# Optimization experiments

Measured on AMD Instinct MI355X. Metric: run time of the kernel, lower is better.

The kernel has to match this reference:

```python
import jax, jax.numpy as jnp
import numpy as np

B, T, F = 2, 128, 88          # batch, time frames, pitch bins (hard-coded 88)
HIDDEN = 64                    # LSTM input dim
N_UNIT = 64                    # channel dim (= 2 * lstm hidden 32)
N_HEAD = 4
HEAD_DIM = N_UNIT // N_HEAD    # 16
WINDOW = 7
N_LAYERS = 2
DIFF_STEPS = 100
LSTM_H = N_UNIT // 2           # 32 per direction


def setup_inputs() -> dict:
    key = jax.random.key(0)
    ks = jax.random.split(key, 12)
    s = 0.05
    inp = {
        'x': jax.random.normal(ks[0], (B, T * F, HIDDEN), jnp.float32),
        't': jax.random.randint(ks[1], (B,), 0, DIFF_STEPS, jnp.int32),
        # LSTM params, stacked [layer, direction, ...]; layer-1 input dim == 2*LSTM_H == HIDDEN
        'lstm_w_ih': s * jax.random.normal(ks[2], (N_LAYERS, 2, 4 * LSTM_H, HIDDEN), jnp.float32),
        'lstm_w_hh': s * jax.random.normal(ks[3], (N_LAYERS, 2, 4 * LSTM_H, LSTM_H), jnp.float32),
        'lstm_b_ih': s * jax.random.normal(ks[4], (N_LAYERS, 2, 4 * LSTM_H), jnp.float32),
        'lstm_b_hh': s * jax.random.normal(ks[5], (N_LAYERS, 2, 4 * LSTM_H), jnp.float32),
        # per-NA-layer params
        't_emb': s * jax.random.normal(ks[6], (N_LAYERS, DIFF_STEPS, N_UNIT), jnp.float32),
        'w_qkv': s * jax.random.normal(ks[7], (N_LAYERS, N_UNIT, 3 * N_UNIT), jnp.float32),
        'b_qkv': jnp.zeros((N_LAYERS, 3 * N_UNIT), jnp.float32),
        'rpb': s * jax.random.normal(ks[8], (N_LAYERS, N_HEAD, 2 * WINDOW - 1, 2 * WINDOW - 1), jnp.float32),
        'w_proj': s * jax.random.normal(ks[9], (N_LAYERS, N_UNIT, N_UNIT), jnp.float32),
        'b_proj': jnp.zeros((N_LAYERS, N_UNIT), jnp.float32),
    }
    return inp


def _lstm_dir(x, w_ih, w_hh, b_ih, b_hh, reverse):
    # x: [N, T, D]; pytorch gate order i, f, g, o
    N = x.shape[0]
    H = w_hh.shape[1]
    xs = jnp.swapaxes(x, 0, 1)
    if reverse:
        xs = xs[::-1]
    b = b_ih + b_hh
    def step(carry, xt):
        h, c = carry
        g = xt @ w_ih.T + h @ w_hh.T + b
        i, f, gg, o = jnp.split(g, 4, axis=-1)
        c = jax.nn.sigmoid(f) * c + jax.nn.sigmoid(i) * jnp.tanh(gg)
        h = jax.nn.sigmoid(o) * jnp.tanh(c)
        return (h, c), h
    h0 = jnp.zeros((N, H), x.dtype)
    _, hs = jax.lax.scan(step, (h0, h0), xs)
    if reverse:
        hs = hs[::-1]
    return jnp.swapaxes(hs, 0, 1)


def _bilstm(x, w_ih, w_hh, b_ih, b_hh):
    for l in range(w_ih.shape[0]):
        fwd = _lstm_dir(x, w_ih[l, 0], w_hh[l, 0], b_ih[l, 0], b_hh[l, 0], False)
        bwd = _lstm_dir(x, w_ih[l, 1], w_hh[l, 1], b_ih[l, 1], b_hh[l, 1], True)
        x = jnp.concatenate([fwd, bwd], axis=-1)
    return x


def _nbh(L, w):
    # NATTEN-style clamped (non-shrinking) neighborhood window per axis
    i = jnp.arange(L)
    start = jnp.clip(i - w // 2, 0, L - w)
    idx = start[:, None] + jnp.arange(w)[None, :]   # [L, w] absolute neighbor idx
    rel = idx - i[:, None] + (w - 1)                # [L, w] rel-pos-bias idx in [0, 2w-2]
    return idx, rel


def _na2d(x, t_idx, emb, wqkv, bqkv, rpb_l, wproj, bproj):
    # x: [B, Th, Tw, C]; diffusion-step conditioning via learned embedding add
    Bx, Th, Tw, C = x.shape
    h = x + emb[t_idx][:, None, None, :]
    qkv = (h @ wqkv + bqkv).reshape(Bx, Th, Tw, 3, N_HEAD, HEAD_DIM)
    q = jnp.moveaxis(qkv[..., 0, :, :], 3, 1) * (HEAD_DIM ** -0.5)  # [B,h,Th,Tw,d]
    k = jnp.moveaxis(qkv[..., 1, :, :], 3, 1)
    v = jnp.moveaxis(qkv[..., 2, :, :], 3, 1)
    ih, rh = _nbh(Th, WINDOW)
    iw, rw = _nbh(Tw, WINDOW)
    # gather windowed neighbors: [B,h,Th,Tw,w,w,d]
    kn = k[:, :, ih[:, None, :, None], iw[None, :, None, :], :]
    vn = v[:, :, ih[:, None, :, None], iw[None, :, None, :], :]
    bias = rpb_l[:, rh[:, None, :, None], rw[None, :, None, :]]     # [h,Th,Tw,w,w]
    logits = jnp.einsum('bhijd,bhijkld->bhijkl', q, kn) + bias[None]
    attn = jax.nn.softmax(logits.reshape(Bx, N_HEAD, Th, Tw, -1), axis=-1).reshape(logits.shape)
    out = jnp.einsum('bhijkl,bhijkld->bhijd', attn, vn)             # [B,h,Th,Tw,d]
    out = jnp.moveaxis(out, 1, 3).reshape(Bx, Th, Tw, C)
    return out @ wproj + bproj


def reference(x, t, lstm_w_ih, lstm_w_hh, lstm_b_ih, lstm_b_hh,
              t_emb, w_qkv, b_qkv, rpb, w_proj, b_proj):
    Bx = x.shape[0]
    Hin = x.shape[-1]
    Tt = x.shape[1] // F
    h = x.reshape(Bx, Tt, F, Hin).transpose(0, 2, 1, 3).reshape(Bx * F, Tt, Hin)
    h = _bilstm(h, lstm_w_ih, lstm_w_hh, lstm_b_ih, lstm_b_hh)      # [B*88, T, n_unit]
    # -> [B, T, 88, n_unit] 2D grid (height=T, width=88)
    h = h.reshape(Bx, F, Tt, N_UNIT).transpose(0, 2, 1, 3)
    for l in range(N_LAYERS):
        h = h + _na2d(h, t, t_emb[l], w_qkv[l], b_qkv[l], rpb[l], w_proj[l], b_proj[l])
    return h
```

## Files before the change

### kernel.cpp

```cpp
#include <hip/hip_runtime.h>
#include <math.h>

#define B_ 2
#define T_ 128
#define F_ 88
#define HID 64
#define NU 64
#define NH 4
#define HD 16
#define LH 32
#define NSEQ (B_*F_)
#define NTOK (B_*T_*F_)
#define NPOS (T_*F_)

__device__ __forceinline__ float fsig(float x) {
    return __builtin_amdgcn_rcpf(1.0f + __expf(-x));
}
__device__ __forceinline__ float ftanh(float x) {
    return 2.0f * __builtin_amdgcn_rcpf(1.0f + __expf(-2.0f*x)) - 1.0f;
}

template<int LAYER>
__global__ void __launch_bounds__(256, 2) gg_kernel(
    const float* __restrict__ xin,
    const float* __restrict__ w_ih,
    const float* __restrict__ b_ih,
    const float* __restrict__ b_hh,
    float* __restrict__ G)
{
    __shared__ __align__(16) float xts[32][68];
    __shared__ __align__(16) float wsh[256][68];
    __shared__ float bsh[256];
    const int s  = blockIdx.x;
    const int t0 = blockIdx.y * 32;
    const int b = s / F_, f = s % F_;
    const int tid = threadIdx.x;

    for (int n = tid; n < 32*64; n += 256) {
        const int tt = n >> 6, k = n & 63;
        xts[tt][k] = (LAYER == 0)
            ? xin[(((size_t)b*T_ + t0+tt)*F_ + f)*HID + k]
            : xin[((size_t)s*T_ + t0+tt)*HID + k];
    }
    for (int n = tid; n < 256*64; n += 256) {
        const int row = n >> 6, k = n & 63;
        wsh[row][k] = w_ih[((size_t)LAYER*256 + row)*HID + k];
    }
    bsh[tid] = b_ih[LAYER*256 + tid] + b_hh[LAYER*256 + tid];
    __syncthreads();

    const int lane = tid & 63;
    const int g    = tid >> 6;
    const int dir  = g >> 1;
    const int th   = g & 1;
    const int rowA = dir*128 + lane;
    const int rowB = dir*128 + 64 + lane;

    float accA[16] = {}, accB[16] = {};
    #pragma unroll 4
    for (int k4 = 0; k4 < 16; k4++) {
        const float4 wA = *(const float4*)&wsh[rowA][k4*4];
        const float4 wB = *(const float4*)&wsh[rowB][k4*4];
        #pragma unroll
        for (int tt = 0; tt < 16; tt++) {
            const float4 xv = *(const float4*)&xts[th*16+tt][k4*4];
            accA[tt] += wA.x*xv.x + wA.y*xv.y + wA.z*xv.z + wA.w*xv.w;
            accB[tt] += wB.x*xv.x + wB.y*xv.y + wB.z*xv.z + wB.w*xv.w;
        }
    }
    const float bA = bsh[rowA], bB = bsh[rowB];
    float2* gout = (float2*)G + ((size_t)(s*2+dir)*T_ + t0 + th*16)*64 + lane;
    #pragma unroll
    for (int tt = 0; tt < 16; tt++) {
        float2 o; o.x = accA[tt] + bA; o.y = accB[tt] + bB;
        gout[(size_t)tt*64] = o;
    }
}

template<int LAYER>
__global__ void __launch_bounds__(128, 1) lstm_rec(
    const float* __restrict__ G,
    const float* __restrict__ w_hh,
    float* __restrict__ outp)
{
    __shared__ float hbuf[T_][NU];
    __shared__ __align__(16) float hstage[2][LH];
    const int s = blockIdx.x;
    const int b = s / F_, f = s % F_;
    const int lane = threadIdx.x & 63;
    const int dir  = threadIdx.x >> 6;

    float2 wh2[LH];
    {
        const float4* pa = (const float4*)(w_hh + ((size_t)(LAYER*2+dir)*128 + lane)*LH);
        const float4* pb = (const float4*)(w_hh + ((size_t)(LAYER*2+dir)*128 + 64 + lane)*LH);
        #pragma unroll
        for (int k4 = 0; k4 < LH/4; k4++) {
            float4 a = pa[k4], c4 = pb[k4];
            wh2[k4*4+0].x=a.x; wh2[k4*4+0].y=c4.x;
            wh2[k4*4+1].x=a.y; wh2[k4*4+1].y=c4.y;
            wh2[k4*4+2].x=a.z; wh2[k4*4+2].y=c4.z;
            wh2[k4*4+3].x=a.w; wh2[k4*4+3].y=c4.w;
        }
    }
    const float2* gp = (const float2*)G + (size_t)(s*2+dir)*T_*64 + lane;
    #define GTIME(st) (dir ? (T_-1-(st)) : (st))

    const float a1 = (lane < LH) ? 2.f : 1.f;
    const float c1 = (lane < LH) ? -1.f : 0.f;

    float h = 0.f, c = 0.f;
    if (lane < LH) hstage[dir][lane] = 0.f;

    #define STEP(gAv, gBv, stepi)                                            \
    {                                                                        \
        float hbc[LH];                                                       \
        _Pragma("unroll")                                                    \
        for (int q = 0; q < LH/4; q++) {                                     \
            const float4 hv = *(const float4*)&hstage[dir][q*4];             \
            hbc[q*4+0]=hv.x; hbc[q*4+1]=hv.y;                                \
            hbc[q*4+2]=hv.z; hbc[q*4+3]=hv.w;                                \
        }                                                                    \
        float aA0 = (gAv), aB0 = (gBv), aA1 = 0.f, aB1 = 0.f;                \
        _Pragma("unroll")                                                    \
        for (int k = 0; k < 16; k++) {                                       \
            aA0 += wh2[k].x*hbc[k];      aB0 += wh2[k].y*hbc[k];             \
            aA1 += wh2[k+16].x*hbc[k+16]; aB1 += wh2[k+16].y*hbc[k+16];      \
        }                                                                    \
        const float accA = aA0 + aA1, accB = aB0 + aB1;                      \
        const float e0 = fsig(accA);                                         \
        const float e1 = fmaf(a1, fsig(a1*accB), c1);                        \
        const float x0 = __shfl_xor(e0, 32, 64);                             \
        const float x1 = __shfl_xor(e1, 32, 64);                             \
        c = x0*c + e0*e1;                                                    \
        h = x1 * ftanh(c);                                                   \
        if (lane < LH) {                                                     \
            hbuf[GTIME(stepi)][dir*LH + lane] = h;                           \
            hstage[dir][lane] = h;                                           \
        }                                                                    \
    }

    float2 A[4], Bf[4];
    #pragma unroll
    for (int i = 0; i < 4; i++) A[i]  = gp[(size_t)GTIME(i)*64];
    #pragma unroll
    for (int i = 0; i < 4; i++) Bf[i] = gp[(size_t)GTIME(4+i)*64];

    #pragma unroll 1
    for (int grp = 0; grp < 32; grp++) {
        float2 P[4];
        const int pf = (grp < 30 ? grp + 2 : 31) * 4;
        #pragma unroll
        for (int i = 0; i < 4; i++) P[i] = gp[(size_t)GTIME(pf+i)*64];
        #pragma unroll
        for (int i = 0; i < 4; i++) { STEP(A[i].x, A[i].y, grp*4 + i); }
        #pragma unroll
        for (int i = 0; i < 4; i++) { A[i] = Bf[i]; Bf[i] = P[i]; }
    }
    #undef STEP
    #undef GTIME
    __syncthreads();

    const int tid = threadIdx.x;
    const float4* lds4 = (const float4*)&hbuf[0][0];
    if (LAYER == 0) {
        float4* out4 = (float4*)outp + (size_t)s*T_*16;
        #pragma unroll
        for (int it = 0; it < 16; it++)
            out4[it*128 + tid] = lds4[it*128 + tid];
    } else {
        const int c4 = tid & 15, trow = tid >> 4;
        #pragma unroll
        for (int it = 0; it < 16; it++) {
            const int t = it*8 + trow;
            ((float4*)outp)[(((size_t)b*T_ + t)*F_ + f)*16 + c4] = lds4[t*16 + c4];
        }
    }
}

__global__ void __launch_bounds__(256, 2) qkv_kernel(
    const float* __restrict__ hcur,
    const int*   __restrict__ tarr,
    const float* __restrict__ t_emb,
    const float* __restrict__ w_qkv,
    const float* __restrict__ b_qkv,
    const int layer,
    float* __restrict__ qb, float* __restrict__ kb, float* __restrict__ vb)
{
    __shared__ float as[64][65];
    __shared__ float wsh[64][64];
    const int m0 = blockIdx.x * 64;
    const int which = blockIdx.y;
    const int tid = threadIdx.x;
    const int bidx = m0 / NPOS;
    const int tb = tarr[bidx];
    const float* embp = t_emb + ((size_t)layer*100 + tb)*HID;

    for (int n = tid; n < 64*64; n += 256) {
        const int mm = n >> 6, k = n & 63;
        as[mm][k]  = hcur[((size_t)m0+mm)*64 + k] + embp[k];
        wsh[mm][k] = w_qkv[((size_t)layer*64 + mm)*192 + which*64 + k];
    }
    __syncthreads();

    const int tm = tid >> 4, tn = tid & 15;
    float acc[4][4] = {};
    for (int k = 0; k < 64; k++) {
        const float a0 = as[tm*4+0][k];
        const float a1 = as[tm*4+1][k];
        const float a2 = as[tm*4+2][k];
        const float a3 = as[tm*4+3][k];
        const float4 w = *(const float4*)&wsh[k][tn*4];
        acc[0][0]+=a0*w.x; acc[0][1]+=a0*w.y; acc[0][2]+=a0*w.z; acc[0][3]+=a0*w.w;
        acc[1][0]+=a1*w.x; acc[1][1]+=a1*w.y; acc[1][2]+=a1*w.z; acc[1][3]+=a1*w.w;
        acc[2][0]+=a2*w.x; acc[2][1]+=a2*w.y; acc[2][2]+=a2*w.z; acc[2][3]+=a2*w.w;
        acc[3][0]+=a3*w.x; acc[3][1]+=a3*w.y; acc[3][2]+=a3*w.z; acc[3][3]+=a3*w.w;
    }

    float* dst = (which == 0) ? qb : (which == 1) ? kb : vb;
    const float scale = (which == 0) ? 0.25f : 1.0f;
    const int hh = tn >> 2;
    const int dbase = (tn & 3) * 4;
    const float4 bv = *(const float4*)&b_qkv[(size_t)layer*192 + which*64 + tn*4];
    #pragma unroll
    for (int r = 0; r < 4; r++) {
        const int row = m0 + tm*4 + r;
        const int pos = row - bidx*NPOS;
        float4 o;
        o.x = (acc[r][0] + bv.x) * scale;
        o.y = (acc[r][1] + bv.y) * scale;
        o.z = (acc[r][2] + bv.z) * scale;
        o.w = (acc[r][3] + bv.w) * scale;
        *(float4*)&dst[(((size_t)bidx*NH + hh)*NPOS + pos)*HD + dbase] = o;
    }
}

__global__ void __launch_bounds__(384, 1) nattn_kernel(
    const float* __restrict__ qb,
    const float* __restrict__ kb,
    const float* __restrict__ vb,
    const float* __restrict__ rpb,
    const int layer,
    float* __restrict__ ao)
{
    __shared__ float kv[2][10][88][20];
    __shared__ float rp[169];
    const int blk = blockIdx.x;
    const int bh = blk & 7;
    const int it = blk >> 3;
    const int i0 = it*4;
    const int h  = bh & 3;
    const int bb = bh >> 2;
    const int tid = threadIdx.x;
    const int rs = min(max(i0-3, 0), T_-10);
    const float* kbase = kb + (size_t)bh*NPOS*HD;
    const float* vbase = vb + (size_t)bh*NPOS*HD;

    const bool act = (tid < 4*F_);
    const int isub = act ? (tid / F_) : 0;
    const int j    = act ? (tid - isub*F_) : 0;
    const int i    = i0 + isub;
    const int ihs  = min(max(i-3, 0), T_-7);
    const int ro   = ihs - rs;
    const int cw   = min(max(j-3, 0), F_-7);

    float4 q0, q1, q2, q3;
    if (act) {
        const float4* qp = (const float4*)&qb[((size_t)bh*NPOS + i*F_ + j)*HD];
        q0 = qp[0]; q1 = qp[1]; q2 = qp[2]; q3 = qp[3];
    }
    for (int n = tid; n < 169; n += 384)
        rp[n] = rpb[((size_t)layer*NH + h)*169 + n];
    for (int n4 = tid; n4 < 10*88*4; n4 += 384) {
        const int d4   = n4 & 3;
        const int rest = n4 >> 2;
        const int c    = rest % 88;
        const int r    = rest / 88;
        const size_t goff = ((size_t)(rs+r)*F_ + c)*HD + d4*4;
        *(float4*)&kv[0][r][c][d4*4] = *(const float4*)&kbase[goff];
        *(float4*)&kv[1][r][c][d4*4] = *(const float4*)&vbase[goff];
    }
    __syncthreads();

    if (act) {
        float lg[49];
        #pragma unroll
        for (int ki = 0; ki < 7; ki++) {
            const int rh = ihs + ki - i + 6;
            #pragma unroll
            for (int kj = 0; kj < 7; kj++) {
                const float4* kp = (const float4*)&kv[0][ro+ki][cw+kj][0];
                const float4 k0 = kp[0], k1 = kp[1], k2 = kp[2], k3 = kp[3];
                float d = q0.x*k0.x + q0.y*k0.y + q0.z*k0.z + q0.w*k0.w
                        + q1.x*k1.x + q1.y*k1.y + q1.z*k1.z + q1.w*k1.w
                        + q2.x*k2.x + q2.y*k2.y + q2.z*k2.z + q2.w*k2.w
                        + q3.x*k3.x + q3.y*k3.y + q3.z*k3.z + q3.w*k3.w;
                lg[ki*7+kj] = d + rp[rh*13 + (cw + kj - j + 6)];
            }
        }
        float m = lg[0];
        #pragma unroll
        for (int n = 1; n < 49; n++) m = fmaxf(m, lg[n]);
        float ssum = 0.f;
        #pragma unroll
        for (int n = 0; n < 49; n++) { lg[n] = __expf(lg[n] - m); ssum += lg[n]; }
        const float inv = __builtin_amdgcn_rcpf(ssum);
        #pragma unroll
        for (int n = 0; n < 49; n++) lg[n] *= inv;

        float4 o0 = {0,0,0,0}, o1 = {0,0,0,0}, o2 = {0,0,0,0}, o3 = {0,0,0,0};
        #pragma unroll
        for (int ki = 0; ki < 7; ki++) {
            #pragma unroll
            for (int kj = 0; kj < 7; kj++) {
                const float a = lg[ki*7+kj];
                const float4* vp = (const float4*)&kv[1][ro+ki][cw+kj][0];
                const float4 v0 = vp[0], v1 = vp[1], v2 = vp[2], v3 = vp[3];
                o0.x += a*v0.x; o0.y += a*v0.y; o0.z += a*v0.z; o0.w += a*v0.w;
                o1.x += a*v1.x; o1.y += a*v1.y; o1.z += a*v1.z; o1.w += a*v1.w;
                o2.x += a*v2.x; o2.y += a*v2.y; o2.z += a*v2.z; o2.w += a*v2.w;
                o3.x += a*v3.x; o3.y += a*v3.y; o3.z += a*v3.z; o3.w += a*v3.w;
            }
        }
        float4* op = (float4*)&ao[(((size_t)bb*T_ + i)*F_ + j)*NU + h*HD];
        op[0]=o0; op[1]=o1; op[2]=o2; op[3]=o3;
    }
}

__global__ void __launch_bounds__(256, 2) proj_kernel(
    const float* __restrict__ ain,
    const float* __restrict__ hres,
    const float* __restrict__ w_proj,
    const float* __restrict__ b_proj,
    const int layer,
    float* __restrict__ outp)
{
    __shared__ float as[64][65];
    __shared__ float wsh[64][64];
    const int m0 = blockIdx.x * 64;
    const int tid = threadIdx.x;
    for (int n = tid; n < 64*64; n += 256) {
        const int mm = n >> 6, k = n & 63;
        as[mm][k]  = ain[((size_t)m0+mm)*64 + k];
        wsh[mm][k] = w_proj[(size_t)layer*4096 + n];
    }
    __syncthreads();
    const int tm = tid >> 4, tn = tid & 15;
    float acc[4][4] = {};
    for (int k = 0; k < 64; k++) {
        const float a0 = as[tm*4+0][k];
        const float a1 = as[tm*4+1][k];
        const float a2 = as[tm*4+2][k];
        const float a3 = as[tm*4+3][k];
        const float4 w = *(const float4*)&wsh[k][tn*4];
        acc[0][0]+=a0*w.x; acc[0][1]+=a0*w.y; acc[0][2]+=a0*w.z; acc[0][3]+=a0*w.w;
        acc[1][0]+=a1*w.x; acc[1][1]+=a1*w.y; acc[1][2]+=a1*w.z; acc[1][3]+=a1*w.w;
        acc[2][0]+=a2*w.x; acc[2][1]+=a2*w.y; acc[2][2]+=a2*w.z; acc[2][3]+=a2*w.w;
        acc[3][0]+=a3*w.x; acc[3][1]+=a3*w.y; acc[3][2]+=a3*w.z; acc[3][3]+=a3*w.w;
    }
    const float4 bv = *(const float4*)&b_proj[(size_t)layer*64 + tn*4];
    #pragma unroll
    for (int r = 0; r < 4; r++) {
        const int row = m0 + tm*4 + r;
        const float4 hv = *(const float4*)&hres[(size_t)row*64 + tn*4];
        float4 o;
        o.x = hv.x + acc[r][0] + bv.x;
        o.y = hv.y + acc[r][1] + bv.y;
        o.z = hv.z + acc[r][2] + bv.z;
        o.w = hv.w + acc[r][3] + bv.w;
        *(float4*)&outp[(size_t)row*64 + tn*4] = o;
    }
}

extern "C" void kernel_launch(void* const* d_in, const int* in_sizes, int n_in,
                              void* d_out, int out_size, void* d_ws, size_t ws_size,
                              hipStream_t stream) {
    const float* x      = (const float*)d_in[0];
    const int*   tarr   = (const int*)  d_in[1];
    const float* w_ih   = (const float*)d_in[2];
    const float* w_hh   = (const float*)d_in[3];
    const float* b_ih   = (const float*)d_in[4];
    const float* b_hh   = (const float*)d_in[5];
    const float* t_emb  = (const float*)d_in[6];
    const float* w_qkv  = (const float*)d_in[7];
    const float* b_qkv  = (const float*)d_in[8];
    const float* rpb    = (const float*)d_in[9];
    const float* w_proj = (const float*)d_in[10];
    const float* b_proj = (const float*)d_in[11];

    float* ws   = (float*)d_ws;
    const size_t CH = (size_t)NTOK * NU;
    float* hcur = ws;
    float* h0   = ws + CH;
    float* G    = ws + 2*CH;
    float* qbuf = ws + 2*CH;
    float* kbuf = ws + 3*CH;
    float* vbuf = ws + 4*CH;
    float* ao   = ws + 5*CH;
    float* outp = (float*)d_out;

    gg_kernel<0><<<dim3(NSEQ, T_/32), 256, 0, stream>>>(x,  w_ih, b_ih, b_hh, G);
    lstm_rec<0><<<NSEQ, 128, 0, stream>>>(G, w_hh, h0);
    gg_kernel<1><<<dim3(NSEQ, T_/32), 256, 0, stream>>>(h0, w_ih, b_ih, b_hh, G);
    lstm_rec<1><<<NSEQ, 128, 0, stream>>>(G, w_hh, hcur);

    for (int l = 0; l < 2; l++) {
        qkv_kernel<<<dim3(NTOK/64, 3), 256, 0, stream>>>(
            hcur, tarr, t_emb, w_qkv, b_qkv, l, qbuf, kbuf, vbuf);
        nattn_kernel<<<(T_/4)*8, 384, 0, stream>>>(
            qbuf, kbuf, vbuf, rpb, l, ao);
        proj_kernel<<<NTOK/64, 256, 0, stream>>>(
            ao, hcur, w_proj, b_proj, l, (l == 0) ? hcur : outp);
    }
}
```

Measured before the change: 241.3 us.

## Fuse LSTM input projection into recurrent kernel with pipelined x staging

Removes the separate gate-precompute kernel and its G buffer round trip through global memory. Each recurrent block now keeps its w_ih rows in registers (128 extra floats per thread) and computes the input projection for future timesteps inside the loop. It stages x through a 4-slot shared ring with one-group-ahead global prefetch, so this work can overlap the serial recurrence. The cost is much higher register pressure and extra ALU work on the latency-bound recurrent path, which runs with only 176 blocks.

```diff
diff --git a/kernel.cpp b/kernel.cpp
--- a/kernel.cpp
+++ b/kernel.cpp
@@ -21,74 +21,37 @@
 }
 
 template<int LAYER>
-__global__ void __launch_bounds__(256, 2) gg_kernel(
+__global__ void __launch_bounds__(128, 1) lstm_fused(
     const float* __restrict__ xin,
     const float* __restrict__ w_ih,
+    const float* __restrict__ w_hh,
     const float* __restrict__ b_ih,
     const float* __restrict__ b_hh,
-    float* __restrict__ G)
-{
-    __shared__ __align__(16) float xts[32][68];
-    __shared__ __align__(16) float wsh[256][68];
-    __shared__ float bsh[256];
-    const int s  = blockIdx.x;
-    const int t0 = blockIdx.y * 32;
-    const int b = s / F_, f = s % F_;
-    const int tid = threadIdx.x;
-
-    for (int n = tid; n < 32*64; n += 256) {
-        const int tt = n >> 6, k = n & 63;
-        xts[tt][k] = (LAYER == 0)
-            ? xin[(((size_t)b*T_ + t0+tt)*F_ + f)*HID + k]
-            : xin[((size_t)s*T_ + t0+tt)*HID + k];
-    }
-    for (int n = tid; n < 256*64; n += 256) {
-        const int row = n >> 6, k = n & 63;
-        wsh[row][k] = w_ih[((size_t)LAYER*256 + row)*HID + k];
-    }
-    bsh[tid] = b_ih[LAYER*256 + tid] + b_hh[LAYER*256 + tid];
-    __syncthreads();
-
-    const int lane = tid & 63;
-    const int g    = tid >> 6;
-    const int dir  = g >> 1;
-    const int th   = g & 1;
-    const int rowA = dir*128 + lane;
-    const int rowB = dir*128 + 64 + lane;
-
-    float accA[16] = {}, accB[16] = {};
-    #pragma unroll 4
-    for (int k4 = 0; k4 < 16; k4++) {
-        const float4 wA = *(const float4*)&wsh[rowA][k4*4];
-        const float4 wB = *(const float4*)&wsh[rowB][k4*4];
-        #pragma unroll
-        for (int tt = 0; tt < 16; tt++) {
-            const float4 xv = *(const float4*)&xts[th*16+tt][k4*4];
-            accA[tt] += wA.x*xv.x + wA.y*xv.y + wA.z*xv.z + wA.w*xv.w;
-            accB[tt] += wB.x*xv.x + wB.y*xv.y + wB.z*xv.z + wB.w*xv.w;
-        }
-    }
-    const float bA = bsh[rowA], bB = bsh[rowB];
-    float2* gout = (float2*)G + ((size_t)(s*2+dir)*T_ + t0 + th*16)*64 + lane;
-    #pragma unroll
-    for (int tt = 0; tt < 16; tt++) {
-        float2 o; o.x = accA[tt] + bA; o.y = accB[tt] + bB;
-        gout[(size_t)tt*64] = o;
-    }
-}
-
-template<int LAYER>
-__global__ void __launch_bounds__(128, 1) lstm_rec(
-    const float* __restrict__ G,
-    const float* __restrict__ w_hh,
     float* __restrict__ outp)
 {
     __shared__ float hbuf[T_][NU];
     __shared__ __align__(16) float hstage[2][LH];
+    __shared__ __align__(16) float xstage[2][4][4][64];
     const int s = blockIdx.x;
     const int b = s / F_, f = s % F_;
     const int lane = threadIdx.x & 63;
     const int dir  = threadIdx.x >> 6;
+
+    float wA[64], wB[64];
+    {
+        const float* wbase = w_ih + (size_t)((LAYER*2+dir)*128)*HID;
+        const float4* pa = (const float4*)(wbase + (size_t)lane*HID);
+        const float4* pb = (const float4*)(wbase + (size_t)(64+lane)*HID);
+        #pragma unroll
+        for (int q = 0; q < 16; q++) {
+            float4 a = pa[q], bq = pb[q];
+            wA[q*4+0]=a.x;  wA[q*4+1]=a.y;  wA[q*4+2]=a.z;  wA[q*4+3]=a.w;
+            wB[q*4+0]=bq.x; wB[q*4+1]=bq.y; wB[q*4+2]=bq.z; wB[q*4+3]=bq.w;
+        }
+    }
+    const int brow = (LAYER*2+dir)*128;
+    const float biasA = b_ih[brow + lane]      + b_hh[brow + lane];
+    const float biasB = b_ih[brow + 64 + lane] + b_hh[brow + 64 + lane];
 
     float2 wh2[LH];
     {
@@ -103,14 +66,41 @@
             wh2[k4*4+3].x=a.w; wh2[k4*4+3].y=c4.w;
         }
     }
-    const float2* gp = (const float2*)G + (size_t)(s*2+dir)*T_*64 + lane;
-    #define GTIME(st) (dir ? (T_-1-(st)) : (st))
 
     const float a1 = (lane < LH) ? 2.f : 1.f;
     const float c1 = (lane < LH) ? -1.f : 0.f;
-
     float h = 0.f, c = 0.f;
     if (lane < LH) hstage[dir][lane] = 0.f;
+
+    #define GTIME(st) (dir ? (T_-1-(st)) : (st))
+    const int xtt = lane >> 4;
+    const int xk4 = (lane & 15) * 4;
+    #define XADDR(t) ((LAYER==0) ? ((((size_t)b*T_+(t))*F_ + f)*HID + xk4) \
+                                 : (((size_t)s*T_+(t))*HID + xk4))
+    #define LOADX(g) (*(const float4*)&xin[XADDR(GTIME(min((g)*4+xtt, T_-1)))])
+    #define STOREX(slot, v) { *(float4*)&xstage[dir][slot][xtt][xk4] = (v); }
+
+    #define PRODUCE(slot, GA, GB)                                            \
+    {                                                                        \
+        _Pragma("unroll")                                                    \
+        for (int tt = 0; tt < 4; tt++) {                                     \
+            float pa0 = biasA, pb0 = biasB, pa1 = 0.f, pb1 = 0.f;            \
+            _Pragma("unroll")                                                \
+            for (int q = 0; q < 8; q++) {                                    \
+                const float4 xv = *(const float4*)&xstage[dir][slot][tt][q*8];   \
+                const float4 xw = *(const float4*)&xstage[dir][slot][tt][q*8+4]; \
+                pa0 += wA[q*8+0]*xv.x + wA[q*8+1]*xv.y                       \
+                     + wA[q*8+2]*xv.z + wA[q*8+3]*xv.w;                      \
+                pb0 += wB[q*8+0]*xv.x + wB[q*8+1]*xv.y                       \
+                     + wB[q*8+2]*xv.z + wB[q*8+3]*xv.w;                      \
+                pa1 += wA[q*8+4]*xw.x + wA[q*8+5]*xw.y                       \
+                     + wA[q*8+6]*xw.z + wA[q*8+7]*xw.w;                      \
+                pb1 += wB[q*8+4]*xw.x + wB[q*8+5]*xw.y                       \
+                     + wB[q*8+6]*xw.z + wB[q*8+7]*xw.w;                      \
+            }                                                                \
+            GA[tt] = pa0 + pa1; GB[tt] = pb0 + pb1;                          \
+        }                                                                    \
+    }
 
     #define STEP(gAv, gBv, stepi)                                            \
     {                                                                        \
@@ -140,24 +130,33 @@
         }                                                                    \
     }
 
-    float2 A[4], Bf[4];
-    #pragma unroll
-    for (int i = 0; i < 4; i++) A[i]  = gp[(size_t)GTIME(i)*64];
-    #pragma unroll
-    for (int i = 0; i < 4; i++) Bf[i] = gp[(size_t)GTIME(4+i)*64];
+    {
+        float4 t0 = LOADX(0), t1 = LOADX(1), t2 = LOADX(2);
+        STOREX(0, t0); STOREX(1, t1); STOREX(2, t2);
+    }
+    float AA[4], AB[4], BA[4], BB[4];
+    PRODUCE(0, AA, AB);
+    PRODUCE(1, BA, BB);
+    float4 xreg = LOADX(3);
 
     #pragma unroll 1
     for (int grp = 0; grp < 32; grp++) {
-        float2 P[4];
-        const int pf = (grp < 30 ? grp + 2 : 31) * 4;
-        #pragma unroll
-        for (int i = 0; i < 4; i++) P[i] = gp[(size_t)GTIME(pf+i)*64];
-        #pragma unroll
-        for (int i = 0; i < 4; i++) { STEP(A[i].x, A[i].y, grp*4 + i); }
-        #pragma unroll
-        for (int i = 0; i < 4; i++) { A[i] = Bf[i]; Bf[i] = P[i]; }
+        STOREX((grp+3)&3, xreg);
+        float PA[4], PB[4];
+        PRODUCE((grp+2)&3, PA, PB);
+        xreg = LOADX(grp+4 < 32 ? grp+4 : 31);
+        #pragma unroll
+        for (int i = 0; i < 4; i++) { STEP(AA[i], AB[i], grp*4 + i); }
+        #pragma unroll
+        for (int i = 0; i < 4; i++) {
+            AA[i]=BA[i]; AB[i]=BB[i]; BA[i]=PA[i]; BB[i]=PB[i];
+        }
     }
     #undef STEP
+    #undef PRODUCE
+    #undef STOREX
+    #undef LOADX
+    #undef XADDR
     #undef GTIME
     __syncthreads();
 
@@ -392,17 +391,14 @@
     const size_t CH = (size_t)NTOK * NU;
     float* hcur = ws;
     float* h0   = ws + CH;
-    float* G    = ws + 2*CH;
     float* qbuf = ws + 2*CH;
     float* kbuf = ws + 3*CH;
     float* vbuf = ws + 4*CH;
     float* ao   = ws + 5*CH;
     float* outp = (float*)d_out;
 
-    gg_kernel<0><<<dim3(NSEQ, T_/32), 256, 0, stream>>>(x,  w_ih, b_ih, b_hh, G);
-    lstm_rec<0><<<NSEQ, 128, 0, stream>>>(G, w_hh, h0);
-    gg_kernel<1><<<dim3(NSEQ, T_/32), 256, 0, stream>>>(h0, w_ih, b_ih, b_hh, G);
-    lstm_rec<1><<<NSEQ, 128, 0, stream>>>(G, w_hh, hcur);
+    lstm_fused<0><<<NSEQ, 128, 0, stream>>>(x,  w_ih, w_hh, b_ih, b_hh, h0);
+    lstm_fused<1><<<NSEQ, 128, 0, stream>>>(h0, w_ih, w_hh, b_ih, b_hh, hcur);
 
     for (int l = 0; l < 2; l++) {
         qkv_kernel<<<dim3(NTOK/64, 3), 256, 0, stream>>>(
```

Result: slower. 627.3 us (+160.0%).
